# Kernel tuning notes

Measured on AMD Instinct MI355X. Metric: run time of the kernel, lower is better.

Reference implementation:

```python
import jax, jax.numpy as jnp
import numpy as np

IN_DIM = 128
NUM_KERNELS = 512
OUT_DIM = 256
EPS_NORM = 1e-09


def setup_inputs() -> dict:
    key = jax.random.key(0)
    k1, k2, k3, k4 = jax.random.split(key, 4)
    inp = jax.random.normal(k1, (16, 512, IN_DIM), dtype=jnp.float32)
    # centers ~ U[-1, 1] as in reset(upper_bound_kernels=1.0)
    centers = jax.random.uniform(k2, (NUM_KERNELS, IN_DIM), dtype=jnp.float32, minval=-1.0, maxval=1.0)
    # log shapes ~ N(0, 0.1)
    log_shapes = 0.1 * jax.random.normal(k3, (NUM_KERNELS,), dtype=jnp.float32)
    # xavier-uniform weights, gain=1: bound = sqrt(6/(fan_in+fan_out))
    bound = float(np.sqrt(6.0 / (NUM_KERNELS + OUT_DIM)))
    weights = jax.random.uniform(k4, (OUT_DIM, NUM_KERNELS), dtype=jnp.float32, minval=-bound, maxval=bound)
    return {"input": inp, "kernels_centers": centers, "log_shapes": log_shapes, "weights": weights}


def reference(input, kernels_centers, log_shapes, weights):
    lead = input.shape[:-1]
    x = input.reshape(-1, input.shape[-1])            # (N, D)
    diff = x[:, None, :] - kernels_centers[None, :, :]  # (N, K, D)
    r = jnp.linalg.norm(diff, axis=-1)                 # (N, K)
    eps_r = jnp.exp(log_shapes)[None, :] * r           # (N, K)
    rbfs = jnp.exp(-eps_r ** 2)                        # gaussian RBF
    rbfs = rbfs / (jnp.sum(rbfs, axis=-1, keepdims=True) + EPS_NORM)
    out = rbfs @ weights.T                             # (N, OUT)
    return out.reshape(lead + (weights.shape[0],))
```

## Files before the change

### kernel.cpp

```cpp
#include <hip/hip_runtime.h>

typedef float  f32x4 __attribute__((ext_vector_type(4)));
typedef short  s16x8 __attribute__((ext_vector_type(8)));
typedef ushort u16x8 __attribute__((ext_vector_type(8)));

constexpr int D  = 128;
constexpr int K  = 512;
constexpr int O  = 256;
constexpr int NT = 256;
constexpr float NL2E = -1.44269504088896340736f;

__device__ __forceinline__ ushort f2bf(float f) {
    uint u = __builtin_bit_cast(uint, f);
    return (ushort)((u + 0x7FFFu + ((u >> 16) & 1u)) >> 16);
}
__device__ __forceinline__ float bf2f(ushort h) {
    return __builtin_bit_cast(float, ((uint)h) << 16);
}

__global__ __launch_bounds__(NT)
void rbf_prep(const float* __restrict__ x, const float* __restrict__ cen,
              const float* __restrict__ ls, const float* __restrict__ w,
              ushort* __restrict__ Xh, ushort* __restrict__ Xl,
              ushort* __restrict__ Ch, ushort* __restrict__ Cl,
              ushort* __restrict__ Wf, float* __restrict__ xs2,
              float2* __restrict__ ecs, int nxb, int ncb)
{
    __shared__ float red[4][16];
    const int b = blockIdx.x, t = threadIdx.x, lane = t & 63, wq = t >> 6;

    if (b < nxb + ncb) {
        const bool isX  = b < nxb;
        const int panel = isX ? b : (b - nxb);
        const float* src = isX ? x : cen;
        ushort* dh = isX ? Xh : Ch;
        ushort* dl = isX ? Xl : Cl;
        const int row = panel * 16 + (lane & 15);
        const int col = wq * 32 + (lane >> 4) * 8;
        const float* p = src + (size_t)row * D + col;
        float4 v0 = *(const float4*)p, v1 = *(const float4*)(p + 4);
        float f[8] = {v0.x, v0.y, v0.z, v0.w, v1.x, v1.y, v1.z, v1.w};
        u16x8 h, l;
        float s = 0.f;
#pragma unroll
        for (int j = 0; j < 8; ++j) {
            s = fmaf(f[j], f[j], s);
            ushort hb = f2bf(f[j]);
            h[j] = hb;
            l[j] = f2bf(f[j] - bf2f(hb));
        }
        const size_t c = ((size_t)panel * 4 + wq) * 64 + lane;
        *(u16x8*)&dh[c * 8] = h;
        *(u16x8*)&dl[c * 8] = l;
        s += __shfl_xor(s, 16);
        s += __shfl_xor(s, 32);
        if (lane < 16) red[wq][lane] = s;
        __syncthreads();
        if (t < 16) {
            float sum = red[0][t] + red[1][t] + red[2][t] + red[3][t];
            if (isX) {
                xs2[panel * 16 + t] = sum;
            } else {
                int k = panel * 16 + t;
                float e = __expf(2.0f * ls[k]);
                ecs[k] = make_float2(NL2E * e, NL2E * e * sum);
            }
        }
    } else {
        const int c0 = (b - nxb - ncb) * NT + t;
        const int ln = c0 & 63, ot = (c0 >> 6) & 15, ks = c0 >> 10;
        const int o  = ot * 16 + (ln & 15);
        const int kb = ks * 32 + (ln >> 4) * 8;
        const float* p = w + (size_t)o * K + kb;
        float4 v0 = *(const float4*)p, v1 = *(const float4*)(p + 4);
        u16x8 h;
        h[0] = f2bf(v0.x); h[1] = f2bf(v0.y); h[2] = f2bf(v0.z); h[3] = f2bf(v0.w);
        h[4] = f2bf(v1.x); h[5] = f2bf(v1.y); h[6] = f2bf(v1.z); h[7] = f2bf(v1.w);
        *(u16x8*)&Wf[(size_t)c0 * 8] = h;
    }
}

constexpr int PP = 40;

__global__ __launch_bounds__(512, 2)
void rbf_main8(const ushort* __restrict__ Xh, const ushort* __restrict__ Xl,
               const ushort* __restrict__ Ch, const ushort* __restrict__ Cl,
               const ushort* __restrict__ Wf, const float* __restrict__ xs2,
               const float2* __restrict__ ecs, float* __restrict__ out, int N)
{
    __shared__ ushort Ps[8][16][PP];
    __shared__ float  Acc[4][16][O + 4];
    __shared__ float  Ls[8][16];

    const int t = threadIdx.x, lane = t & 63, wv = t >> 6;
    const int l15 = lane & 15, l4 = lane >> 4;
    const int pan = blockIdx.x;

    s16x8 xh[4], xl[4];
    {
        const size_t base = ((size_t)pan * 4) * 64 + lane;
#pragma unroll
        for (int q = 0; q < 4; ++q) {
            xh[q] = *(const s16x8*)&Xh[(base + q * 64) * 8];
            xl[q] = *(const s16x8*)&Xl[(base + q * 64) * 8];
        }
    }
    const float xs2v = xs2[pan * 16 + l15];

    f32x4 oacc[16];
#pragma unroll
    for (int i = 0; i < 16; ++i) oacc[i] = (f32x4){0.f, 0.f, 0.f, 0.f};
    float Lp = 0.f;

    const int kw = wv * 64;

#pragma unroll
    for (int s = 0; s < 2; ++s) {
        const int kslab = (kw >> 5) + s;
        const ushort* wbase = &Wf[(((size_t)kslab * 16) * 64 + lane) * 8];

#pragma unroll
        for (int bt = 0; bt < 2; ++bt) {
            const size_t kt16 = (size_t)(kw >> 4) + s * 2 + bt;
            s16x8 ch[4], cl[4];
#pragma unroll
            for (int q = 0; q < 4; ++q) {
                const size_t cc = ((kt16 * 4 + q) * 64 + lane) * 8;
                ch[q] = *(const s16x8*)&Ch[cc];
                cl[q] = *(const s16x8*)&Cl[cc];
            }
            f32x4 ghh = (f32x4){0.f,0.f,0.f,0.f};
            f32x4 ghl = (f32x4){0.f,0.f,0.f,0.f};
            f32x4 glh = (f32x4){0.f,0.f,0.f,0.f};
#pragma unroll
            for (int q = 0; q < 4; ++q) {
                ghh = __builtin_amdgcn_mfma_f32_16x16x32_bf16(ch[q], xh[q], ghh, 0, 0, 0);
                ghl = __builtin_amdgcn_mfma_f32_16x16x32_bf16(ch[q], xl[q], ghl, 0, 0, 0);
                glh = __builtin_amdgcn_mfma_f32_16x16x32_bf16(cl[q], xh[q], glh, 0, 0, 0);
            }
            f32x4 g = ghh + ghl + glh;

            const int kbase = kw + s * 32 + bt * 16 + l4 * 4;
            float4 e0 = *(const float4*)&ecs[kbase];
            float4 e1 = *(const float4*)&ecs[kbase + 2];
            float ph0 = exp2f(fmaf(e0.x, fmaf(-2.f, g[0], xs2v), e0.y));
            float ph1 = exp2f(fmaf(e0.z, fmaf(-2.f, g[1], xs2v), e0.w));
            float ph2 = exp2f(fmaf(e1.x, fmaf(-2.f, g[2], xs2v), e1.y));
            float ph3 = exp2f(fmaf(e1.z, fmaf(-2.f, g[3], xs2v), e1.w));
            Lp += (ph0 + ph1) + (ph2 + ph3);
            uint p0 = (uint)f2bf(ph0) | ((uint)f2bf(ph1) << 16);
            uint p1 = (uint)f2bf(ph2) | ((uint)f2bf(ph3) << 16);
            *(uint2*)&Ps[wv][l15][bt * 16 + l4 * 4] = make_uint2(p0, p1);
        }

        s16x8 pa = *(const s16x8*)&Ps[wv][l15][l4 * 8];
#pragma unroll
        for (int ot = 0; ot < 16; ++ot) {
            s16x8 bfr = *(const s16x8*)&wbase[(size_t)ot * 64 * 8];
            oacc[ot] = __builtin_amdgcn_mfma_f32_16x16x32_bf16(pa, bfr, oacc[ot], 0, 0, 0);
        }
    }

    {
        float v = Lp;
        v += __shfl_xor(v, 16);
        v += __shfl_xor(v, 32);
        if (lane < 16) Ls[wv][lane] = v;
    }

    if (wv < 4) {
#pragma unroll
        for (int ot = 0; ot < 16; ++ot)
#pragma unroll
            for (int r = 0; r < 4; ++r)
                Acc[wv][l4 * 4 + r][ot * 16 + l15] = oacc[ot][r];
    }
    __syncthreads();
    if (wv >= 4) {
#pragma unroll
        for (int ot = 0; ot < 16; ++ot)
#pragma unroll
            for (int r = 0; r < 4; ++r)
                Acc[wv - 4][l4 * 4 + r][ot * 16 + l15] += oacc[ot][r];
    }
    __syncthreads();

    {
        const int n  = t >> 5;
        const int c8 = (t & 31) * 8;
        float inv = 1.0f / (Ls[0][n] + Ls[1][n] + Ls[2][n] + Ls[3][n] +
                            Ls[4][n] + Ls[5][n] + Ls[6][n] + Ls[7][n] + 1e-9f);
        float4 a0 = *(const float4*)&Acc[0][n][c8];
        float4 b0 = *(const float4*)&Acc[1][n][c8];
        float4 c0 = *(const float4*)&Acc[2][n][c8];
        float4 d0 = *(const float4*)&Acc[3][n][c8];
        float4 a1 = *(const float4*)&Acc[0][n][c8 + 4];
        float4 b1 = *(const float4*)&Acc[1][n][c8 + 4];
        float4 c1 = *(const float4*)&Acc[2][n][c8 + 4];
        float4 d1 = *(const float4*)&Acc[3][n][c8 + 4];
        float4 o0, o1;
        o0.x = ((a0.x + b0.x) + (c0.x + d0.x)) * inv;
        o0.y = ((a0.y + b0.y) + (c0.y + d0.y)) * inv;
        o0.z = ((a0.z + b0.z) + (c0.z + d0.z)) * inv;
        o0.w = ((a0.w + b0.w) + (c0.w + d0.w)) * inv;
        o1.x = ((a1.x + b1.x) + (c1.x + d1.x)) * inv;
        o1.y = ((a1.y + b1.y) + (c1.y + d1.y)) * inv;
        o1.z = ((a1.z + b1.z) + (c1.z + d1.z)) * inv;
        o1.w = ((a1.w + b1.w) + (c1.w + d1.w)) * inv;
        float* po = &out[(size_t)(pan * 16 + n) * O + c8];
        *(float4*)po = o0;
        *(float4*)(po + 4) = o1;
    }
}

__global__ __launch_bounds__(NT, 2)
void rbf_fb(const float* __restrict__ x, const float* __restrict__ cen,
            const float* __restrict__ ls, const float* __restrict__ w,
            float* __restrict__ out)
{
    __shared__ ushort Ps2[2][4][16][PP];
    __shared__ float  Acc2[2][16][O + 4];
    __shared__ float  Ls2[4][16];
    const int t = threadIdx.x, lane = t & 63, wv = t >> 6;
    const int l15 = lane & 15, l4 = lane >> 4;
    const int nb = blockIdx.x * 16;

    s16x8 xh[4], xl[4];
    float sx = 0.f;
    {
        const float* xr = x + (size_t)(nb + l15) * D;
#pragma unroll
        for (int q = 0; q < 4; ++q) {
            float4 v0 = *(const float4*)(xr + q * 32 + l4 * 8);
            float4 v1 = *(const float4*)(xr + q * 32 + l4 * 8 + 4);
            float f[8] = {v0.x, v0.y, v0.z, v0.w, v1.x, v1.y, v1.z, v1.w};
            s16x8 hh, lo;
#pragma unroll
            for (int j = 0; j < 8; ++j) {
                sx = fmaf(f[j], f[j], sx);
                ushort hb = f2bf(f[j]);
                hh[j] = (short)hb; lo[j] = (short)f2bf(f[j] - bf2f(hb));
            }
            xh[q] = hh; xl[q] = lo;
        }
    }
    sx += __shfl_xor(sx, 16); sx += __shfl_xor(sx, 32);
    float xs2v[4];
#pragma unroll
    for (int r = 0; r < 4; ++r) xs2v[r] = __shfl(sx, l4 * 4 + r);

    f32x4 oacc[16];
#pragma unroll
    for (int ot = 0; ot < 16; ++ot) oacc[ot] = (f32x4){0.f,0.f,0.f,0.f};
    float Lp[4] = {0.f,0.f,0.f,0.f};
    const int kq = wv * (K / 4);

#pragma unroll
    for (int s = 0; s < 4; ++s) {
        const int k0 = kq + s * 32;
#pragma unroll
        for (int bt = 0; bt < 2; ++bt) {
            const int kk = k0 + bt * 16 + l15;
            const float* cr = cen + (size_t)kk * D;
            s16x8 ch[4], cl[4];
            float sc = 0.f;
#pragma unroll
            for (int q = 0; q < 4; ++q) {
                float4 v0 = *(const float4*)(cr + q * 32 + l4 * 8);
                float4 v1 = *(const float4*)(cr + q * 32 + l4 * 8 + 4);
                float f[8] = {v0.x, v0.y, v0.z, v0.w, v1.x, v1.y, v1.z, v1.w};
                s16x8 hh, lo;
#pragma unroll
                for (int j = 0; j < 8; ++j) {
                    sc = fmaf(f[j], f[j], sc);
                    ushort hb = f2bf(f[j]);
                    hh[j] = (short)hb; lo[j] = (short)f2bf(f[j] - bf2f(hb));
                }
                ch[q] = hh; cl[q] = lo;
            }
            sc += __shfl_xor(sc, 16); sc += __shfl_xor(sc, 32);
            float es_ = __expf(2.0f * ls[kk]);
            f32x4 ghh={0,0,0,0}, ghl={0,0,0,0}, glh={0,0,0,0};
#pragma unroll
            for (int q = 0; q < 4; ++q) {
                ghh = __builtin_amdgcn_mfma_f32_16x16x32_bf16(xh[q], ch[q], ghh, 0,0,0);
                ghl = __builtin_amdgcn_mfma_f32_16x16x32_bf16(xh[q], cl[q], ghl, 0,0,0);
                glh = __builtin_amdgcn_mfma_f32_16x16x32_bf16(xl[q], ch[q], glh, 0,0,0);
            }
            f32x4 gg = ghh + ghl + glh;
#pragma unroll
            for (int r = 0; r < 4; ++r) {
                float r2 = xs2v[r] + sc - 2.0f * gg[r];
                float ph = __expf(-es_ * r2);
                Lp[r] += ph;
                Ps2[s & 1][wv][l4 * 4 + r][bt * 16 + l15] = f2bf(ph);
            }
        }
        s16x8 pa = *(const s16x8*)&Ps2[s & 1][wv][l15][l4 * 8];
#pragma unroll
        for (int ot = 0; ot < 16; ++ot) {
            const float* wr = w + (size_t)(ot * 16 + l15) * K + k0;
            float4 v0 = *(const float4*)(wr + l4 * 8);
            float4 v1 = *(const float4*)(wr + l4 * 8 + 4);
            s16x8 bb;
            bb[0]=(short)f2bf(v0.x); bb[1]=(short)f2bf(v0.y); bb[2]=(short)f2bf(v0.z); bb[3]=(short)f2bf(v0.w);
            bb[4]=(short)f2bf(v1.x); bb[5]=(short)f2bf(v1.y); bb[6]=(short)f2bf(v1.z); bb[7]=(short)f2bf(v1.w);
            oacc[ot] = __builtin_amdgcn_mfma_f32_16x16x32_bf16(pa, bb, oacc[ot], 0,0,0);
        }
    }
#pragma unroll
    for (int r = 0; r < 4; ++r) {
        float v = Lp[r];
        v += __shfl_xor(v, 1); v += __shfl_xor(v, 2);
        v += __shfl_xor(v, 4); v += __shfl_xor(v, 8);
        if (l15 == 0) Ls2[wv][l4 * 4 + r] = v;
    }
    if (wv < 2) {
#pragma unroll
        for (int ot = 0; ot < 16; ++ot)
#pragma unroll
            for (int r = 0; r < 4; ++r)
                Acc2[wv][l4 * 4 + r][ot * 16 + l15] = oacc[ot][r];
    }
    __syncthreads();
    if (wv >= 2) {
#pragma unroll
        for (int ot = 0; ot < 16; ++ot)
#pragma unroll
            for (int r = 0; r < 4; ++r)
                Acc2[wv - 2][l4 * 4 + r][ot * 16 + l15] += oacc[ot][r];
    }
    __syncthreads();
#pragma unroll
    for (int rr = 0; rr < 4; ++rr) {
        const int n = wv * 4 + rr;
        float inv = 1.0f / (Ls2[0][n] + Ls2[1][n] + Ls2[2][n] + Ls2[3][n] + 1e-9f);
        float4 a0 = *(const float4*)&Acc2[0][n][lane * 4];
        float4 a1 = *(const float4*)&Acc2[1][n][lane * 4];
        float4 o4;
        o4.x = (a0.x + a1.x) * inv; o4.y = (a0.y + a1.y) * inv;
        o4.z = (a0.z + a1.z) * inv; o4.w = (a0.w + a1.w) * inv;
        *(float4*)&out[(size_t)(nb + n) * O + lane * 4] = o4;
    }
}

extern "C" void kernel_launch(void* const* d_in, const int* in_sizes, int n_in,
                              void* d_out, int out_size, void* d_ws, size_t ws_size,
                              hipStream_t stream) {
    const float* x   = (const float*)d_in[0];
    const float* cen = (const float*)d_in[1];
    const float* ls  = (const float*)d_in[2];
    const float* w   = (const float*)d_in[3];
    float* out = (float*)d_out;
    const int N = in_sizes[0] / D;

    size_t oXh = 0;
    size_t oXl = oXh + (size_t)N * D * 2;
    size_t oCh = oXl + (size_t)N * D * 2;
    size_t oCl = oCh + (size_t)K * D * 2;
    size_t oWf = oCl + (size_t)K * D * 2;
    size_t oxs = oWf + (size_t)O * K * 2;
    size_t oec = oxs + (size_t)N * 4;
    size_t need = oec + (size_t)K * 8;

    if (ws_size < need || (N % 16) != 0) {
        dim3 grid(N / 16), block(NT);
        hipLaunchKernelGGL(rbf_fb, grid, block, 0, stream, x, cen, ls, w, out);
        return;
    }

    char* ws = (char*)d_ws;
    ushort* Xh = (ushort*)(ws + oXh);
    ushort* Xl = (ushort*)(ws + oXl);
    ushort* Ch = (ushort*)(ws + oCh);
    ushort* Cl = (ushort*)(ws + oCl);
    ushort* Wf = (ushort*)(ws + oWf);
    float*  xs2 = (float*)(ws + oxs);
    float2* ecs = (float2*)(ws + oec);

    const int nxb = N / 16;
    const int ncb = K / 16;
    const int nwb = (O * K / 8) / NT;
    dim3 pgrid(nxb + ncb + nwb), pblock(NT);
    hipLaunchKernelGGL(rbf_prep, pgrid, pblock, 0, stream,
                       x, cen, ls, w, Xh, Xl, Ch, Cl, Wf, xs2, ecs, nxb, ncb);

    dim3 grid(N / 16), block(512);
    hipLaunchKernelGGL(rbf_main8, grid, block, 0, stream,
                       Xh, Xl, Ch, Cl, Wf, xs2, ecs, out, N);
}
```

Before: 27.44 us.

## Process two 16-row panels per block to reuse center and weight fragments

The main kernel now handles 32 rows per block as two 16-row panels. It interleaves the MFMAs for both panels so each loaded center and weight fragment is used twice, and the grid shrinks to N/32 blocks. The cross-wave accumulator reduction becomes a four-stage serialized add into two slices. The change halves global reads of C and W per row and gives the MFMA pipe independent chains to overlap. In exchange it roughly doubles register use (launch bounds drop to 1 block per CU), leaves only 256 blocks, and adds more __syncthreads.

```diff
diff --git a/kernel.cpp b/kernel.cpp
--- a/kernel.cpp
+++ b/kernel.cpp
@@ -82,35 +82,43 @@
 
 constexpr int PP = 40;
 
-__global__ __launch_bounds__(512, 2)
-void rbf_main8(const ushort* __restrict__ Xh, const ushort* __restrict__ Xl,
-               const ushort* __restrict__ Ch, const ushort* __restrict__ Cl,
-               const ushort* __restrict__ Wf, const float* __restrict__ xs2,
-               const float2* __restrict__ ecs, float* __restrict__ out, int N)
+__global__ __launch_bounds__(512, 1)
+void rbf_main2p(const ushort* __restrict__ Xh, const ushort* __restrict__ Xl,
+                const ushort* __restrict__ Ch, const ushort* __restrict__ Cl,
+                const ushort* __restrict__ Wf, const float* __restrict__ xs2,
+                const float2* __restrict__ ecs, float* __restrict__ out, int N)
 {
-    __shared__ ushort Ps[8][16][PP];
-    __shared__ float  Acc[4][16][O + 4];
-    __shared__ float  Ls[8][16];
+    __shared__ ushort PsA[8][16][PP];
+    __shared__ ushort PsB[8][16][PP];
+    __shared__ float  Acc[2][32][O + 4];
+    __shared__ float  Ls[8][32];
 
     const int t = threadIdx.x, lane = t & 63, wv = t >> 6;
     const int l15 = lane & 15, l4 = lane >> 4;
     const int pan = blockIdx.x;
 
-    s16x8 xh[4], xl[4];
+    s16x8 xhA[4], xlA[4], xhB[4], xlB[4];
     {
-        const size_t base = ((size_t)pan * 4) * 64 + lane;
+        const size_t baseA = ((size_t)(pan * 2) * 4) * 64 + lane;
+        const size_t baseB = ((size_t)(pan * 2 + 1) * 4) * 64 + lane;
 #pragma unroll
         for (int q = 0; q < 4; ++q) {
-            xh[q] = *(const s16x8*)&Xh[(base + q * 64) * 8];
-            xl[q] = *(const s16x8*)&Xl[(base + q * 64) * 8];
-        }
-    }
-    const float xs2v = xs2[pan * 16 + l15];
-
-    f32x4 oacc[16];
-#pragma unroll
-    for (int i = 0; i < 16; ++i) oacc[i] = (f32x4){0.f, 0.f, 0.f, 0.f};
-    float Lp = 0.f;
+            xhA[q] = *(const s16x8*)&Xh[(baseA + q * 64) * 8];
+            xlA[q] = *(const s16x8*)&Xl[(baseA + q * 64) * 8];
+            xhB[q] = *(const s16x8*)&Xh[(baseB + q * 64) * 8];
+            xlB[q] = *(const s16x8*)&Xl[(baseB + q * 64) * 8];
+        }
+    }
+    const float xs2A = xs2[pan * 32 + l15];
+    const float xs2B = xs2[pan * 32 + 16 + l15];
+
+    f32x4 oaccA[16], oaccB[16];
+#pragma unroll
+    for (int i = 0; i < 16; ++i) {
+        oaccA[i] = (f32x4){0.f, 0.f, 0.f, 0.f};
+        oaccB[i] = (f32x4){0.f, 0.f, 0.f, 0.f};
+    }
+    float LpA = 0.f, LpB = 0.f;
 
     const int kw = wv * 64;
 
@@ -129,87 +137,127 @@
                 ch[q] = *(const s16x8*)&Ch[cc];
                 cl[q] = *(const s16x8*)&Cl[cc];
             }
-            f32x4 ghh = (f32x4){0.f,0.f,0.f,0.f};
-            f32x4 ghl = (f32x4){0.f,0.f,0.f,0.f};
-            f32x4 glh = (f32x4){0.f,0.f,0.f,0.f};
-#pragma unroll
-            for (int q = 0; q < 4; ++q) {
-                ghh = __builtin_amdgcn_mfma_f32_16x16x32_bf16(ch[q], xh[q], ghh, 0, 0, 0);
-                ghl = __builtin_amdgcn_mfma_f32_16x16x32_bf16(ch[q], xl[q], ghl, 0, 0, 0);
-                glh = __builtin_amdgcn_mfma_f32_16x16x32_bf16(cl[q], xh[q], glh, 0, 0, 0);
-            }
-            f32x4 g = ghh + ghl + glh;
+            f32x4 gA = (f32x4){0.f,0.f,0.f,0.f};
+            f32x4 gB = (f32x4){0.f,0.f,0.f,0.f};
+#pragma unroll
+            for (int q = 0; q < 4; ++q) {
+                gA = __builtin_amdgcn_mfma_f32_16x16x32_bf16(ch[q], xhA[q], gA, 0, 0, 0);
+                gB = __builtin_amdgcn_mfma_f32_16x16x32_bf16(ch[q], xhB[q], gB, 0, 0, 0);
+            }
+#pragma unroll
+            for (int q = 0; q < 4; ++q) {
+                gA = __builtin_amdgcn_mfma_f32_16x16x32_bf16(ch[q], xlA[q], gA, 0, 0, 0);
+                gB = __builtin_amdgcn_mfma_f32_16x16x32_bf16(ch[q], xlB[q], gB, 0, 0, 0);
+            }
+#pragma unroll
+            for (int q = 0; q < 4; ++q) {
+                gA = __builtin_amdgcn_mfma_f32_16x16x32_bf16(cl[q], xhA[q], gA, 0, 0, 0);
+                gB = __builtin_amdgcn_mfma_f32_16x16x32_bf16(cl[q], xhB[q], gB, 0, 0, 0);
+            }
 
             const int kbase = kw + s * 32 + bt * 16 + l4 * 4;
             float4 e0 = *(const float4*)&ecs[kbase];
             float4 e1 = *(const float4*)&ecs[kbase + 2];
-            float ph0 = exp2f(fmaf(e0.x, fmaf(-2.f, g[0], xs2v), e0.y));
-            float ph1 = exp2f(fmaf(e0.z, fmaf(-2.f, g[1], xs2v), e0.w));
-            float ph2 = exp2f(fmaf(e1.x, fmaf(-2.f, g[2], xs2v), e1.y));
-            float ph3 = exp2f(fmaf(e1.z, fmaf(-2.f, g[3], xs2v), e1.w));
-            Lp += (ph0 + ph1) + (ph2 + ph3);
-            uint p0 = (uint)f2bf(ph0) | ((uint)f2bf(ph1) << 16);
-            uint p1 = (uint)f2bf(ph2) | ((uint)f2bf(ph3) << 16);
-            *(uint2*)&Ps[wv][l15][bt * 16 + l4 * 4] = make_uint2(p0, p1);
-        }
-
-        s16x8 pa = *(const s16x8*)&Ps[wv][l15][l4 * 8];
+            {
+                float p0 = exp2f(fmaf(e0.x, fmaf(-2.f, gA[0], xs2A), e0.y));
+                float p1 = exp2f(fmaf(e0.z, fmaf(-2.f, gA[1], xs2A), e0.w));
+                float p2 = exp2f(fmaf(e1.x, fmaf(-2.f, gA[2], xs2A), e1.y));
+                float p3 = exp2f(fmaf(e1.z, fmaf(-2.f, gA[3], xs2A), e1.w));
+                LpA += (p0 + p1) + (p2 + p3);
+                uint u0 = (uint)f2bf(p0) | ((uint)f2bf(p1) << 16);
+                uint u1 = (uint)f2bf(p2) | ((uint)f2bf(p3) << 16);
+                *(uint2*)&PsA[wv][l15][bt * 16 + l4 * 4] = make_uint2(u0, u1);
+            }
+            {
+                float p0 = exp2f(fmaf(e0.x, fmaf(-2.f, gB[0], xs2B), e0.y));
+                float p1 = exp2f(fmaf(e0.z, fmaf(-2.f, gB[1], xs2B), e0.w));
+                float p2 = exp2f(fmaf(e1.x, fmaf(-2.f, gB[2], xs2B), e1.y));
+                float p3 = exp2f(fmaf(e1.z, fmaf(-2.f, gB[3], xs2B), e1.w));
+                LpB += (p0 + p1) + (p2 + p3);
+                uint u0 = (uint)f2bf(p0) | ((uint)f2bf(p1) << 16);
+                uint u1 = (uint)f2bf(p2) | ((uint)f2bf(p3) << 16);
+                *(uint2*)&PsB[wv][l15][bt * 16 + l4 * 4] = make_uint2(u0, u1);
+            }
+        }
+
+        s16x8 paA = *(const s16x8*)&PsA[wv][l15][l4 * 8];
+        s16x8 paB = *(const s16x8*)&PsB[wv][l15][l4 * 8];
 #pragma unroll
         for (int ot = 0; ot < 16; ++ot) {
             s16x8 bfr = *(const s16x8*)&wbase[(size_t)ot * 64 * 8];
-            oacc[ot] = __builtin_amdgcn_mfma_f32_16x16x32_bf16(pa, bfr, oacc[ot], 0, 0, 0);
+            oaccA[ot] = __builtin_amdgcn_mfma_f32_16x16x32_bf16(paA, bfr, oaccA[ot], 0, 0, 0);
+            oaccB[ot] = __builtin_amdgcn_mfma_f32_16x16x32_bf16(paB, bfr, oaccB[ot], 0, 0, 0);
         }
     }
 
     {
-        float v = Lp;
-        v += __shfl_xor(v, 16);
-        v += __shfl_xor(v, 32);
-        if (lane < 16) Ls[wv][lane] = v;
-    }
-
-    if (wv < 4) {
-#pragma unroll
-        for (int ot = 0; ot < 16; ++ot)
-#pragma unroll
-            for (int r = 0; r < 4; ++r)
-                Acc[wv][l4 * 4 + r][ot * 16 + l15] = oacc[ot][r];
-    }
-    __syncthreads();
-    if (wv >= 4) {
-#pragma unroll
-        for (int ot = 0; ot < 16; ++ot)
-#pragma unroll
-            for (int r = 0; r < 4; ++r)
-                Acc[wv - 4][l4 * 4 + r][ot * 16 + l15] += oacc[ot][r];
+        float vA = LpA, vB = LpB;
+        vA += __shfl_xor(vA, 16);  vA += __shfl_xor(vA, 32);
+        vB += __shfl_xor(vB, 16);  vB += __shfl_xor(vB, 32);
+        if (lane < 16) {
+            Ls[wv][lane]      = vA;
+            Ls[wv][16 + lane] = vB;
+        }
+    }
+
+    if (wv < 2) {
+#pragma unroll
+        for (int ot = 0; ot < 16; ++ot)
+#pragma unroll
+            for (int r = 0; r < 4; ++r) {
+                Acc[wv][l4 * 4 + r][ot * 16 + l15]      = oaccA[ot][r];
+                Acc[wv][16 + l4 * 4 + r][ot * 16 + l15] = oaccB[ot][r];
+            }
+    }
+    __syncthreads();
+    if (wv == 2 || wv == 3) {
+#pragma unroll
+        for (int ot = 0; ot < 16; ++ot)
+#pragma unroll
+            for (int r = 0; r < 4; ++r) {
+                Acc[wv - 2][l4 * 4 + r][ot * 16 + l15]      += oaccA[ot][r];
+                Acc[wv - 2][16 + l4 * 4 + r][ot * 16 + l15] += oaccB[ot][r];
+            }
+    }
+    __syncthreads();
+    if (wv == 4 || wv == 5) {
+#pragma unroll
+        for (int ot = 0; ot < 16; ++ot)
+#pragma unroll
+            for (int r = 0; r < 4; ++r) {
+                Acc[wv - 4][l4 * 4 + r][ot * 16 + l15]      += oaccA[ot][r];
+                Acc[wv - 4][16 + l4 * 4 + r][ot * 16 + l15] += oaccB[ot][r];
+            }
+    }
+    __syncthreads();
+    if (wv >= 6) {
+#pragma unroll
+        for (int ot = 0; ot < 16; ++ot)
+#pragma unroll
+            for (int r = 0; r < 4; ++r) {
+                Acc[wv - 6][l4 * 4 + r][ot * 16 + l15]      += oaccA[ot][r];
+                Acc[wv - 6][16 + l4 * 4 + r][ot * 16 + l15] += oaccB[ot][r];
+            }
     }
     __syncthreads();
 
     {
-        const int n  = t >> 5;
-        const int c8 = (t & 31) * 8;
+        const int n  = t >> 4;
+        const int c0 = (t & 15) * 16;
         float inv = 1.0f / (Ls[0][n] + Ls[1][n] + Ls[2][n] + Ls[3][n] +
                             Ls[4][n] + Ls[5][n] + Ls[6][n] + Ls[7][n] + 1e-9f);
-        float4 a0 = *(const float4*)&Acc[0][n][c8];
-        float4 b0 = *(const float4*)&Acc[1][n][c8];
-        float4 c0 = *(const float4*)&Acc[2][n][c8];
-        float4 d0 = *(const float4*)&Acc[3][n][c8];
-        float4 a1 = *(const float4*)&Acc[0][n][c8 + 4];
-        float4 b1 = *(const float4*)&Acc[1][n][c8 + 4];
-        float4 c1 = *(const float4*)&Acc[2][n][c8 + 4];
-        float4 d1 = *(const float4*)&Acc[3][n][c8 + 4];
-        float4 o0, o1;
-        o0.x = ((a0.x + b0.x) + (c0.x + d0.x)) * inv;
-        o0.y = ((a0.y + b0.y) + (c0.y + d0.y)) * inv;
-        o0.z = ((a0.z + b0.z) + (c0.z + d0.z)) * inv;
-        o0.w = ((a0.w + b0.w) + (c0.w + d0.w)) * inv;
-        o1.x = ((a1.x + b1.x) + (c1.x + d1.x)) * inv;
-        o1.y = ((a1.y + b1.y) + (c1.y + d1.y)) * inv;
-        o1.z = ((a1.z + b1.z) + (c1.z + d1.z)) * inv;
-        o1.w = ((a1.w + b1.w) + (c1.w + d1.w)) * inv;
-        float* po = &out[(size_t)(pan * 16 + n) * O + c8];
-        *(float4*)po = o0;
-        *(float4*)(po + 4) = o1;
+        float* po = &out[(size_t)(pan * 32 + n) * O + c0];
+#pragma unroll
+        for (int j = 0; j < 4; ++j) {
+            float4 a = *(const float4*)&Acc[0][n][c0 + j * 4];
+            float4 b = *(const float4*)&Acc[1][n][c0 + j * 4];
+            float4 o;
+            o.x = (a.x + b.x) * inv;
+            o.y = (a.y + b.y) * inv;
+            o.z = (a.z + b.z) * inv;
+            o.w = (a.w + b.w) * inv;
+            *(float4*)(po + j * 4) = o;
+        }
     }
 }
 
@@ -363,7 +411,7 @@
     size_t oec = oxs + (size_t)N * 4;
     size_t need = oec + (size_t)K * 8;
 
-    if (ws_size < need || (N % 16) != 0) {
+    if (ws_size < need || (N % 32) != 0) {
         dim3 grid(N / 16), block(NT);
         hipLaunchKernelGGL(rbf_fb, grid, block, 0, stream, x, cen, ls, w, out);
         return;
@@ -385,7 +433,7 @@
     hipLaunchKernelGGL(rbf_prep, pgrid, pblock, 0, stream,
                        x, cen, ls, w, Xh, Xl, Ch, Cl, Wf, xs2, ecs, nxb, ncb);
 
-    dim3 grid(N / 16), block(512);
-    hipLaunchKernelGGL(rbf_main8, grid, block, 0, stream,
+    dim3 grid(N / 32), block(512);
+    hipLaunchKernelGGL(rbf_main2p, grid, block, 0, stream,
                        Xh, Xl, Ch, Cl, Wf, xs2, ecs, out, N);
 }
```

After: 27.76 us. About the same (+1.2%).
